# Performance work log

Measured on AMD Instinct MI355X. Metric: run time of the kernel, lower is better.

The kernel has to match this reference:

```python
import jax, jax.numpy as jnp
import numpy as np

B, C, T, D = 16, 1024, 2048, 512
EPS = 1e-5


def setup_inputs() -> dict:
    key = jax.random.key(0)
    ks = jax.random.split(key, 11)
    s_c = 1.0 / np.sqrt(C)
    s_d = 1.0 / np.sqrt(D)
    return {
        "x": jax.random.normal(ks[0], (B, C, T), dtype=jnp.float32),
        "Wq": jax.random.uniform(ks[1], (D, C), jnp.float32, -s_c, s_c),
        "bq": jax.random.uniform(ks[2], (D,), jnp.float32, -s_c, s_c),
        "Wk": jax.random.uniform(ks[3], (D, C), jnp.float32, -s_c, s_c),
        "bk": jax.random.uniform(ks[4], (D,), jnp.float32, -s_c, s_c),
        "Wv": jax.random.uniform(ks[5], (D, C), jnp.float32, -s_c, s_c),
        "bv": jax.random.uniform(ks[6], (D,), jnp.float32, -s_c, s_c),
        "Wo": jax.random.uniform(ks[7], (C, D), jnp.float32, -s_d, s_d),
        "bo": jax.random.uniform(ks[8], (C,), jnp.float32, -s_d, s_d),
        "gamma": jax.random.normal(ks[9], (C,), dtype=jnp.float32) * 0.1,
        "beta": jax.random.normal(ks[10], (C,), dtype=jnp.float32) * 0.1,
    }


def reference(x, Wq, bq, Wk, bk, Wv, bv, Wo, bo, gamma, beta):
    b, c, t = x.shape
    d = Wq.shape[0]
    # 1x1 Conv1d projections == channel-wise GEMMs
    q = jnp.einsum('dc,bct->btd', Wq, x) + bq            # (B, T, D)
    k = jnp.einsum('dc,bct->bdt', Wk, x) + bk[None, :, None]  # (B, D, T)
    v = jnp.einsum('dc,bct->bdt', Wv, x) + bv[None, :, None]  # (B, D, T)
    # sub_sample: MaxPool1d(kernel=2) on key/value along time
    k = k.reshape(b, d, t // 2, 2).max(axis=-1)          # (B, D, S)
    v = v.reshape(b, d, t // 2, 2).max(axis=-1)          # (B, D, S)
    # softmax-free attention: (Q @ K) / T then @ V
    attn = jnp.einsum('btd,bds->bts', q, k) / t          # (B, T, S)
    out = jnp.einsum('bts,bds->bdt', attn, v)            # (B, D, T)
    # output 1x1 conv
    y = jnp.einsum('cd,bdt->bct', Wo, out) + bo[None, :, None]  # (B, C, T)
    # BatchNorm1d (training-mode batch stats, biased variance)
    mu = y.mean(axis=(0, 2), keepdims=True)
    var = y.var(axis=(0, 2), keepdims=True)
    y = gamma[None, :, None] * (y - mu) * jax.lax.rsqrt(var + EPS) + beta[None, :, None]
    return y + x
```

## Files before the change

kernel.cpp:

```cpp
#include <hip/hip_runtime.h>

typedef unsigned short ushort_t;
typedef __bf16 bf16x8 __attribute__((ext_vector_type(8)));
typedef float floatx4 __attribute__((ext_vector_type(4)));
typedef ushort_t ushortx8 __attribute__((ext_vector_type(8)));

#define BM 128
#define BN 128
#define BKK 64

__device__ __forceinline__ ushort_t f2bf(float f) {
  union { float f; unsigned int u; } c; c.f = f;
  unsigned int r = c.u + 0x7FFFu + ((c.u >> 16) & 1u);
  return (ushort_t)(r >> 16);
}

__device__ __forceinline__ void async16(const ushort_t* g, ushort_t* l) {
  __builtin_amdgcn_global_load_lds(
      (const __attribute__((address_space(1))) unsigned int*)g,
      (__attribute__((address_space(3))) unsigned int*)l, 16, 0, 0);
}

template<int BIASM, int POOLM, bool OUTF32, bool STATS = false>
__global__ __launch_bounds__(512, 2)
void gemm256(const ushort_t* __restrict__ A, long aStr,
             const ushort_t* __restrict__ B, long bStr,
             void* __restrict__ Cp, long cStr,
             int K, int lda, int ldb, int ldc,
             const float* __restrict__ bias, float scale,
             float2* __restrict__ pstat = nullptr)
{
  __shared__ ushort_t As[2][256][64];
  __shared__ ushort_t Bs[2][256][64];
  __shared__ float2 part[4][256];

  A += (long)blockIdx.z * aStr;
  B += (long)blockIdx.z * bStr;
  float* Cf = (float*)Cp + (OUTF32 ? (long)blockIdx.z * cStr : 0);
  ushort_t* Cb = (ushort_t*)Cp + (OUTF32 ? 0 : (long)blockIdx.z * cStr);
  const int m0 = blockIdx.y * 256;
  const int n0 = blockIdx.x * 256;
  const int tid = threadIdx.x;
  const int lane = tid & 63;
  const int wid = tid >> 6;
  const int wm = wid >> 2;
  const int wn = wid & 3;
  const int l15 = lane & 15;
  const int lq  = lane >> 4;

  const int srow = tid >> 3;
  const int scb  = (((tid & 7) ^ (srow & 7)) << 3);
  const int dcb  = (tid & 7) << 3;

  const ushort_t* gA = A + (long)(m0 + srow) * lda + scb;
  const ushort_t* gB = B + (long)(n0 + srow) * ldb + scb;

  const int pb0 = ((lq ^ (l15 & 7)) << 3);
  const int pb1 = (((4 | lq) ^ (l15 & 7)) << 3);

  floatx4 acc[8][4];
#pragma unroll
  for (int i = 0; i < 8; ++i)
#pragma unroll
    for (int j = 0; j < 4; ++j)
#pragma unroll
      for (int r = 0; r < 4; ++r) acc[i][j][r] = 0.0f;

  bf16x8 aA[4][2], bB0[2][2], bB1[2][2];

  const int NT = K >> 6;
  const int NI = NT >> 1;

#define STAGE_A(sl, hf, kt) do { \
    const ushort_t* _s = gA + (long)((hf) * 128) * lda + ((kt) << 6); \
    async16(_s,                  &As[sl][(hf)*128      + srow][dcb]); \
    async16(_s + (long)64 * lda, &As[sl][(hf)*128 + 64 + srow][dcb]); \
  } while (0)
#define STAGE_B(sl, hf, kt) do { \
    const ushort_t* _s = gB + (long)((hf) * 128) * ldb + ((kt) << 6); \
    async16(_s,                  &Bs[sl][(hf)*128      + srow][dcb]); \
    async16(_s + (long)64 * ldb, &Bs[sl][(hf)*128 + 64 + srow][dcb]); \
  } while (0)
#define LD_A(sl, mh) do { \
    _Pragma("unroll") for (int _i = 0; _i < 4; ++_i) { \
      const int _r = wm*128 + (mh)*64 + _i*16 + l15; \
      aA[_i][0] = *(const bf16x8*)&As[sl][_r][pb0]; \
      aA[_i][1] = *(const bf16x8*)&As[sl][_r][pb1]; } \
  } while (0)
#define LD_B(sl, nh, dst) do { \
    _Pragma("unroll") for (int _j = 0; _j < 2; ++_j) { \
      const int _r = wn*64 + (nh)*32 + _j*16 + l15; \
      dst[_j][0] = *(const bf16x8*)&Bs[sl][_r][pb0]; \
      dst[_j][1] = *(const bf16x8*)&Bs[sl][_r][pb1]; } \
  } while (0)
#define MMA(mh, nh, bfr) do { \
    __builtin_amdgcn_s_setprio(1); \
    _Pragma("unroll") for (int _i = 0; _i < 4; ++_i) \
    _Pragma("unroll") for (int _j = 0; _j < 2; ++_j) { \
      floatx4& _c = acc[(mh)*4 + _i][(nh)*2 + _j]; \
      _c = __builtin_amdgcn_mfma_f32_16x16x32_bf16(aA[_i][0], (bfr)[_j][0], _c, 0, 0, 0); \
      _c = __builtin_amdgcn_mfma_f32_16x16x32_bf16(aA[_i][1], (bfr)[_j][1], _c, 0, 0, 0); } \
    __builtin_amdgcn_s_setprio(0); \
  } while (0)
#define SBAR  __builtin_amdgcn_s_barrier()
#define LGKM0 asm volatile("s_waitcnt lgkmcnt(0)" ::: "memory")
#define VM4   asm volatile("s_waitcnt vmcnt(4)" ::: "memory")
#define VM0   asm volatile("s_waitcnt vmcnt(0)" ::: "memory")

  STAGE_A(0, 0, 0); STAGE_A(0, 1, 0); STAGE_B(0, 0, 0); STAGE_B(0, 1, 0);
  STAGE_A(1, 0, 1); STAGE_B(1, 1, 1);
  VM4; SBAR;

  for (int i = 0; i < NI - 1; ++i) {
    const int t1 = 2*i + 1, t2 = 2*i + 2, t3 = 2*i + 3;
    LD_A(0, 0); LD_B(0, 0, bB0); STAGE_A(1, 1, t1);
    SBAR; LGKM0; MMA(0, 0, bB0); SBAR;
    LD_B(0, 1, bB1); STAGE_B(1, 0, t1);
    SBAR; LGKM0; MMA(0, 1, bB1); SBAR;
    LD_A(0, 1); STAGE_A(0, 0, t2);
    SBAR; LGKM0; MMA(1, 1, bB1); SBAR;
    STAGE_B(0, 1, t2);
    SBAR; LGKM0; MMA(1, 0, bB0); VM4; SBAR;
    LD_A(1, 0); LD_B(1, 0, bB0); STAGE_A(0, 1, t2);
    SBAR; LGKM0; MMA(0, 0, bB0); SBAR;
    LD_B(1, 1, bB1); STAGE_B(0, 0, t2);
    SBAR; LGKM0; MMA(0, 1, bB1); SBAR;
    LD_A(1, 1); STAGE_A(1, 0, t3);
    SBAR; LGKM0; MMA(1, 1, bB1); SBAR;
    STAGE_B(1, 1, t3);
    SBAR; LGKM0; MMA(1, 0, bB0); VM4; SBAR;
  }
  {
    const int t1 = NT - 1;
    LD_A(0, 0); LD_B(0, 0, bB0); STAGE_A(1, 1, t1);
    SBAR; LGKM0; MMA(0, 0, bB0); SBAR;
    LD_B(0, 1, bB1); STAGE_B(1, 0, t1);
    SBAR; LGKM0; MMA(0, 1, bB1); SBAR;
    LD_A(0, 1);
    SBAR; LGKM0; MMA(1, 1, bB1); SBAR;
    SBAR; LGKM0; MMA(1, 0, bB0); VM0; SBAR;
    LD_A(1, 0); LD_B(1, 0, bB0);
    SBAR; LGKM0; MMA(0, 0, bB0); SBAR;
    LD_B(1, 1, bB1);
    SBAR; LGKM0; MMA(0, 1, bB1); SBAR;
    LD_A(1, 1);
    SBAR; LGKM0; MMA(1, 1, bB1); SBAR;
    LGKM0; MMA(1, 0, bB0);
  }
#undef STAGE_A
#undef STAGE_B
#undef LD_A
#undef LD_B
#undef MMA
#undef SBAR
#undef LGKM0
#undef VM4
#undef VM0

#pragma unroll
  for (int mi = 0; mi < 8; ++mi) {
    const int mbase = m0 + wm*128 + (mi >> 2)*64 + (mi & 3)*16 + lq*4;
    float ss[4], ss2[4];
    if (STATS) {
#pragma unroll
      for (int r = 0; r < 4; ++r) { ss[r] = 0.0f; ss2[r] = 0.0f; }
    }
#pragma unroll
    for (int nj = 0; nj < 4; ++nj) {
      const int n = n0 + wn*64 + (nj >> 1)*32 + (nj & 1)*16 + l15;
      float v[4];
#pragma unroll
      for (int r = 0; r < 4; ++r) {
        v[r] = acc[mi][nj][r] * scale;
        if (BIASM == 1) v[r] += bias[mbase + r];
      }
      if (BIASM == 2) {
        const float bn_ = bias[n];
#pragma unroll
        for (int r = 0; r < 4; ++r) v[r] += bn_;
      }
      if (STATS) {
#pragma unroll
        for (int r = 0; r < 4; ++r) { ss[r] += v[r]; ss2[r] += v[r] * v[r]; }
      }
      if (POOLM == 0) {
#pragma unroll
        for (int r = 0; r < 4; ++r) {
          if (OUTF32) Cf[(long)(mbase + r) * ldc + n] = v[r];
          else        Cb[(long)(mbase + r) * ldc + n] = f2bf(v[r]);
        }
      } else if (POOLM == 1) {
#pragma unroll
        for (int r = 0; r < 4; ++r) {
          float o = __shfl_xor(v[r], 1);
          float w = fmaxf(v[r], o);
          if ((lane & 1) == 0) {
            if (OUTF32) Cf[(long)(mbase + r) * ldc + (n >> 1)] = w;
            else        Cb[(long)(mbase + r) * ldc + (n >> 1)] = f2bf(w);
          }
        }
      } else {
        float w0 = fmaxf(v[0], v[1]);
        float w1 = fmaxf(v[2], v[3]);
        const int mh = mbase >> 1;
        if (OUTF32) {
          Cf[(long)mh * ldc + n] = w0;
          Cf[(long)(mh + 1) * ldc + n] = w1;
        } else {
          Cb[(long)mh * ldc + n] = f2bf(w0);
          Cb[(long)(mh + 1) * ldc + n] = f2bf(w1);
        }
      }
    }
    if (STATS) {
#pragma unroll
      for (int o = 1; o < 16; o <<= 1) {
#pragma unroll
        for (int r = 0; r < 4; ++r) {
          ss[r]  += __shfl_xor(ss[r],  o);
          ss2[r] += __shfl_xor(ss2[r], o);
        }
      }
      if (l15 == 0) {
        const int chb = wm*128 + (mi >> 2)*64 + (mi & 3)*16 + lq*4;
#pragma unroll
        for (int r = 0; r < 4; ++r) part[wn][chb + r] = make_float2(ss[r], ss2[r]);
      }
    }
  }
  if (STATS) {
    __syncthreads();
    if (tid < 256) {
      float2 p0 = part[0][tid], p1 = part[1][tid], p2 = part[2][tid], p3 = part[3][tid];
      float2 p = make_float2(p0.x + p1.x + p2.x + p3.x, p0.y + p1.y + p2.y + p3.y);
      pstat[((long)blockIdx.z * gridDim.x + blockIdx.x) * 1024 + m0 + tid] = p;
    }
  }
}

template<int BIASM, int POOLM, bool OUTF32>
__global__ __launch_bounds__(256)
void gemm_bt(const ushort_t* __restrict__ A, long aStr,
             const ushort_t* __restrict__ B, long bStr,
             void* __restrict__ Cp, long cStr,
             int K, int lda, int ldb, int ldc,
             const float* __restrict__ bias, float scale)
{
  __shared__ ushort_t As[BM][BKK];
  __shared__ ushort_t Bs[BN][BKK];
  A += (long)blockIdx.z * aStr;
  B += (long)blockIdx.z * bStr;
  float* Cf = (float*)Cp + (OUTF32 ? (long)blockIdx.z * cStr : 0);
  ushort_t* Cb = (ushort_t*)Cp + (OUTF32 ? 0 : (long)blockIdx.z * cStr);
  const int m0 = blockIdx.y * BM;
  const int n0 = blockIdx.x * BN;
  const int tid = threadIdx.x;
  const int lane = tid & 63;
  const int wm = (tid >> 7) & 1;
  const int wn = (tid >> 6) & 1;
  const int ar = tid >> 3;
  const int ac = (tid & 7) * 8;

  floatx4 acc[4][4];
#pragma unroll
  for (int i = 0; i < 4; ++i)
#pragma unroll
    for (int j = 0; j < 4; ++j)
#pragma unroll
      for (int r = 0; r < 4; ++r) acc[i][j][r] = 0.0f;

  const int q8 = (lane >> 4) * 8;
  const int l15 = lane & 15;

  const ushort_t* gA = &A[(long)(m0 + ar) * lda + ac];
  const ushort_t* gB = &B[(long)(n0 + ar) * ldb + ac];
  const long aRow32 = (long)32 * lda;
  const long bRow32 = (long)32 * ldb;

  for (int k0 = 0; k0 < K; k0 += BKK) {
#pragma unroll
    for (int p = 0; p < 4; ++p)
      async16(gA + p * aRow32 + k0, &As[p * 32 + ar][ac]);
#pragma unroll
    for (int p = 0; p < 4; ++p)
      async16(gB + p * bRow32 + k0, &Bs[p * 32 + ar][ac]);
    __syncthreads();
#pragma unroll
    for (int kk = 0; kk < 2; ++kk) {
      const int kr = kk * 32 + q8;
      bf16x8 af[4], bfr[4];
#pragma unroll
      for (int i = 0; i < 4; ++i) {
        af[i]  = *(const bf16x8*)(&As[wm * 64 + i * 16 + l15][kr]);
        bfr[i] = *(const bf16x8*)(&Bs[wn * 64 + i * 16 + l15][kr]);
      }
#pragma unroll
      for (int i = 0; i < 4; ++i)
#pragma unroll
        for (int j = 0; j < 4; ++j)
          acc[i][j] = __builtin_amdgcn_mfma_f32_16x16x32_bf16(af[i], bfr[j], acc[i][j], 0, 0, 0);
    }
    __syncthreads();
  }

#pragma unroll
  for (int i = 0; i < 4; ++i) {
    const int mbase = m0 + wm * 64 + i * 16 + (lane >> 4) * 4;
#pragma unroll
    for (int j = 0; j < 4; ++j) {
      const int n = n0 + wn * 64 + j * 16 + l15;
      float v[4];
#pragma unroll
      for (int r = 0; r < 4; ++r) {
        v[r] = acc[i][j][r] * scale;
        if (BIASM == 1) v[r] += bias[mbase + r];
      }
      if (BIASM == 2) {
        const float bn_ = bias[n];
#pragma unroll
        for (int r = 0; r < 4; ++r) v[r] += bn_;
      }
      if (POOLM == 0) {
#pragma unroll
        for (int r = 0; r < 4; ++r) {
          if (OUTF32) Cf[(long)(mbase + r) * ldc + n] = v[r];
          else        Cb[(long)(mbase + r) * ldc + n] = f2bf(v[r]);
        }
      } else if (POOLM == 1) {
#pragma unroll
        for (int r = 0; r < 4; ++r) {
          float o = __shfl_xor(v[r], 1);
          float w = fmaxf(v[r], o);
          if ((lane & 1) == 0) {
            if (OUTF32) Cf[(long)(mbase + r) * ldc + (n >> 1)] = w;
            else        Cb[(long)(mbase + r) * ldc + (n >> 1)] = f2bf(w);
          }
        }
      } else {
        float w0 = fmaxf(v[0], v[1]);
        float w1 = fmaxf(v[2], v[3]);
        const int mh = mbase >> 1;
        if (OUTF32) {
          Cf[(long)mh * ldc + n] = w0;
          Cf[(long)(mh + 1) * ldc + n] = w1;
        } else {
          Cb[(long)mh * ldc + n] = f2bf(w0);
          Cb[(long)(mh + 1) * ldc + n] = f2bf(w1);
        }
      }
    }
  }
}

__global__ __launch_bounds__(256)
void transpose_f32_bf16(const float* __restrict__ src, ushort_t* __restrict__ dst,
                        int Rr, int Cl)
{
  __shared__ ushort_t tileT[64][72];
  const long boff = (long)blockIdx.z * Rr * Cl;
  const int t0 = blockIdx.x * 64;
  const int r0 = blockIdx.y * 64;
  const int tx = threadIdx.x & 15;
  const int ty = threadIdx.x >> 4;
#pragma unroll
  for (int i = 0; i < 4; ++i) {
    const int c = ty + 16 * i;
    floatx4 v = *(const floatx4*)&src[boff + (long)(r0 + c) * Cl + t0 + 4 * tx];
#pragma unroll
    for (int j = 0; j < 4; ++j) tileT[4 * tx + j][c] = f2bf(v[j]);
  }
  __syncthreads();
  const int cx = threadIdx.x & 7;
  const int tw = threadIdx.x >> 3;
#pragma unroll
  for (int i = 0; i < 2; ++i) {
    const int t = tw + 32 * i;
    ushortx8 w = *(const ushortx8*)&tileT[t][8 * cx];
    *(ushortx8*)&dst[boff + (long)(t0 + t) * Rr + r0 + 8 * cx] = w;
  }
}

__global__ __launch_bounds__(256)
void convert4(const float* __restrict__ a, const float* __restrict__ b,
              const float* __restrict__ c, const float* __restrict__ d,
              ushort_t* __restrict__ dst, int n,
              const float* __restrict__ bk, const float* __restrict__ bv,
              float* __restrict__ bkv)
{
  const float* srcs[4] = {a, b, c, d};
  const float* s = srcs[blockIdx.y];
  int i = blockIdx.x * 256 + threadIdx.x;
  if (i < n) dst[(long)blockIdx.y * n + i] = f2bf(s[i]);
  if (blockIdx.y == 0 && blockIdx.x == 0) {
    for (int j = threadIdx.x; j < 1024; j += 256)
      bkv[j] = (j < 512) ? bk[j] : bv[j - 512];
  }
}

__global__ __launch_bounds__(256)
void bn_apply(float* __restrict__ y, const float* __restrict__ x,
              const float2* __restrict__ pstat, const float* __restrict__ gamma,
              const float* __restrict__ beta)
{
  const int bc = blockIdx.x;
  const int c = bc & 1023;
  float s = 0.0f, s2 = 0.0f;
  if (threadIdx.x < 128) {
    float2 p = pstat[(long)threadIdx.x * 1024 + c];
    s = p.x; s2 = p.y;
  }
#pragma unroll
  for (int o = 32; o > 0; o >>= 1) { s += __shfl_down(s, o); s2 += __shfl_down(s2, o); }
  __shared__ float red[4];
  __shared__ float smv[2];
  const int w = threadIdx.x >> 6;
  if ((threadIdx.x & 63) == 0 && w < 2) { red[w] = s; red[2 + w] = s2; }
  __syncthreads();
  if (threadIdx.x == 0) {
    float ts = red[0] + red[1], ts2 = red[2] + red[3];
    const float inv = 1.0f / (16.0f * 2048.0f);
    float mean = ts * inv;
    float var = ts2 * inv - mean * mean;
    smv[0] = mean;
    smv[1] = rsqrtf(var + 1e-5f);
  }
  __syncthreads();
  const float mean = smv[0];
  const float g = gamma[c] * smv[1];
  const float bt = beta[c];
  const long off = (long)bc * 2048;
  floatx4* yp = (floatx4*)(y + off);
  const floatx4* xp = (const floatx4*)(x + off);
  for (int t = threadIdx.x; t < 512; t += 256) {
    floatx4 v = yp[t];
    floatx4 xv = xp[t];
#pragma unroll
    for (int r = 0; r < 4; ++r) v[r] = (v[r] - mean) * g + bt + xv[r];
    yp[t] = v;
  }
}

extern "C" void kernel_launch(void* const* d_in, const int* in_sizes, int n_in,
                              void* d_out, int out_size, void* d_ws, size_t ws_size,
                              hipStream_t stream) {
  (void)in_sizes; (void)n_in; (void)out_size; (void)ws_size;
  const float* x  = (const float*)d_in[0];
  const float* Wq = (const float*)d_in[1];
  const float* bq = (const float*)d_in[2];
  const float* Wk = (const float*)d_in[3];
  const float* bk = (const float*)d_in[4];
  const float* Wv = (const float*)d_in[5];
  const float* bv = (const float*)d_in[6];
  const float* Wo = (const float*)d_in[7];
  const float* bo = (const float*)d_in[8];
  const float* gamma = (const float*)d_in[9];
  const float* beta  = (const float*)d_in[10];
  float* out = (float*)d_out;

  const int Cc = 1024, T = 2048, D = 512, S = 1024;

  ushort_t* ws   = (ushort_t*)d_ws;
  ushort_t* xT   = ws;
  ushort_t* Qt   = ws + 33554432;
  ushort_t* KV   = ws + 50331648;
  ushort_t* WtT  = ws + 67108864;
  ushort_t* Wco  = ws + 71303168;
  ushort_t* Wq_b = ws + 79691776;
  ushort_t* Wo_b = ws + 79691776 + 3 * 524288;
  float*    bkv  = (float*)(ws + 81788928);
  float2*   pstat = (float2*)(ws + 81790976);

  dim3 blk(256);
  dim3 blk512(512);

  convert4<<<dim3(2048, 4), blk, 0, stream>>>(Wq, Wk, Wv, Wo, Wq_b, D * Cc,
                                              bk, bv, bkv);

  transpose_f32_bf16<<<dim3(T / 64, Cc / 64, 16), blk, 0, stream>>>(x, xT, Cc, T);

  gemm256<2, 0, false><<<dim3(D / 256, T / 256, 16), blk512, 0, stream>>>(
      xT, (long)T * Cc, Wq_b, 0, Qt, (long)T * D, Cc, Cc, Cc, D, bq, 1.0f);
  gemm256<1, 1, false><<<dim3(T / 256, 2 * D / 256, 16), blk512, 0, stream>>>(
      Wq_b + (long)D * Cc, 0, xT, (long)T * Cc, KV, (long)2 * D * S,
      Cc, Cc, Cc, S, bkv, 1.0f);

  gemm_bt<0, 0, false><<<dim3(D / 128, D / 128, 16), blk, 0, stream>>>(
      KV, (long)2 * D * S, KV + (long)D * S, (long)2 * D * S, WtT, (long)D * D,
      S, S, S, D, nullptr, 1.0f);
  gemm_bt<0, 0, false><<<dim3(D / 128, Cc / 128, 16), blk, 0, stream>>>(
      Wo_b, 0, WtT, (long)D * D, Wco, (long)Cc * D,
      D, D, D, D, nullptr, 1.0f / 2048.0f);

  gemm256<1, 0, true, true><<<dim3(T / 256, Cc / 256, 16), blk512, 0, stream>>>(
      Wco, (long)Cc * D, Qt, (long)T * D, out, (long)Cc * T,
      D, D, D, T, bo, 1.0f, pstat);

  bn_apply<<<dim3(16384), blk, 0, stream>>>(out, x, pstat, gamma, beta);
}
```

Measured before the change: 528.5 us.

## Merge Q/KV projection GEMMs into one launch and store pre-BN output as bf16

The Q projection and the pooled K/V projection now run in a single gemm_qkv launch. Block index picks the branch, and both branches share a factored-out gemm_core main loop. The output GEMM now writes its pre-BatchNorm result to a bf16 workspace buffer instead of f32 in the output tensor, while batch statistics are still taken from the f32 accumulators. bn_apply reads that bf16 buffer and writes the final f32 output, which cuts the traffic of the largest intermediate. The trade-off is extra rounding error from storing y in bf16 before normalization.

Measured after the change: 517.4 us. 2.1% less time.

```diff
diff --git a/kernel.cpp b/kernel.cpp
--- a/kernel.cpp
+++ b/kernel.cpp
@@ -4,6 +4,7 @@
 typedef __bf16 bf16x8 __attribute__((ext_vector_type(8)));
 typedef float floatx4 __attribute__((ext_vector_type(4)));
 typedef ushort_t ushortx8 __attribute__((ext_vector_type(8)));
+typedef ushort_t ushortx4 __attribute__((ext_vector_type(4)));
 
 #define BM 128
 #define BN 128
@@ -15,59 +16,26 @@
   return (ushort_t)(r >> 16);
 }
 
+__device__ __forceinline__ float bf2f(ushort_t u) {
+  union { unsigned int u; float f; } c; c.u = ((unsigned int)u) << 16;
+  return c.f;
+}
+
 __device__ __forceinline__ void async16(const ushort_t* g, ushort_t* l) {
   __builtin_amdgcn_global_load_lds(
       (const __attribute__((address_space(1))) unsigned int*)g,
       (__attribute__((address_space(3))) unsigned int*)l, 16, 0, 0);
 }
 
-template<int BIASM, int POOLM, bool OUTF32, bool STATS = false>
-__global__ __launch_bounds__(512, 2)
-void gemm256(const ushort_t* __restrict__ A, long aStr,
-             const ushort_t* __restrict__ B, long bStr,
-             void* __restrict__ Cp, long cStr,
-             int K, int lda, int ldb, int ldc,
-             const float* __restrict__ bias, float scale,
-             float2* __restrict__ pstat = nullptr)
-{
-  __shared__ ushort_t As[2][256][64];
-  __shared__ ushort_t Bs[2][256][64];
-  __shared__ float2 part[4][256];
-
-  A += (long)blockIdx.z * aStr;
-  B += (long)blockIdx.z * bStr;
-  float* Cf = (float*)Cp + (OUTF32 ? (long)blockIdx.z * cStr : 0);
-  ushort_t* Cb = (ushort_t*)Cp + (OUTF32 ? 0 : (long)blockIdx.z * cStr);
-  const int m0 = blockIdx.y * 256;
-  const int n0 = blockIdx.x * 256;
-  const int tid = threadIdx.x;
-  const int lane = tid & 63;
-  const int wid = tid >> 6;
-  const int wm = wid >> 2;
-  const int wn = wid & 3;
-  const int l15 = lane & 15;
-  const int lq  = lane >> 4;
-
-  const int srow = tid >> 3;
-  const int scb  = (((tid & 7) ^ (srow & 7)) << 3);
-  const int dcb  = (tid & 7) << 3;
-
-  const ushort_t* gA = A + (long)(m0 + srow) * lda + scb;
-  const ushort_t* gB = B + (long)(n0 + srow) * ldb + scb;
-
-  const int pb0 = ((lq ^ (l15 & 7)) << 3);
-  const int pb1 = (((4 | lq) ^ (l15 & 7)) << 3);
-
-  floatx4 acc[8][4];
-#pragma unroll
-  for (int i = 0; i < 8; ++i)
-#pragma unroll
-    for (int j = 0; j < 4; ++j)
-#pragma unroll
-      for (int r = 0; r < 4; ++r) acc[i][j][r] = 0.0f;
-
+__device__ __forceinline__ void gemm_core(
+    const ushort_t* __restrict__ gA, const ushort_t* __restrict__ gB,
+    int lda, int ldb, int K,
+    ushort_t (&As)[2][256][64], ushort_t (&Bs)[2][256][64],
+    const int srow, const int dcb, const int wm, const int wn,
+    const int l15, const int pb0, const int pb1,
+    floatx4 (&acc)[8][4])
+{
   bf16x8 aA[4][2], bB0[2][2], bB1[2][2];
-
   const int NT = K >> 6;
   const int NI = NT >> 1;
 
@@ -156,6 +124,52 @@
 #undef LGKM0
 #undef VM4
 #undef VM0
+}
+
+template<int BIASM, int POOLM, bool OUTF32, bool STATS = false>
+__global__ __launch_bounds__(512, 2)
+void gemm256(const ushort_t* __restrict__ A, long aStr,
+             const ushort_t* __restrict__ B, long bStr,
+             void* __restrict__ Cp, long cStr,
+             int K, int lda, int ldb, int ldc,
+             const float* __restrict__ bias, float scale,
+             float2* __restrict__ pstat = nullptr)
+{
+  __shared__ ushort_t As[2][256][64];
+  __shared__ ushort_t Bs[2][256][64];
+  __shared__ float2 part[4][256];
+
+  A += (long)blockIdx.z * aStr;
+  B += (long)blockIdx.z * bStr;
+  float* Cf = (float*)Cp + (OUTF32 ? (long)blockIdx.z * cStr : 0);
+  ushort_t* Cb = (ushort_t*)Cp + (OUTF32 ? 0 : (long)blockIdx.z * cStr);
+  const int m0 = blockIdx.y * 256;
+  const int n0 = blockIdx.x * 256;
+  const int tid = threadIdx.x;
+  const int lane = tid & 63;
+  const int wid = tid >> 6;
+  const int wm = wid >> 2;
+  const int wn = wid & 3;
+  const int l15 = lane & 15;
+  const int lq  = lane >> 4;
+  const int srow = tid >> 3;
+  const int scb  = (((tid & 7) ^ (srow & 7)) << 3);
+  const int dcb  = (tid & 7) << 3;
+  const int pb0 = ((lq ^ (l15 & 7)) << 3);
+  const int pb1 = (((4 | lq) ^ (l15 & 7)) << 3);
+
+  const ushort_t* gA = A + (long)(m0 + srow) * lda + scb;
+  const ushort_t* gB = B + (long)(n0 + srow) * ldb + scb;
+
+  floatx4 acc[8][4];
+#pragma unroll
+  for (int i = 0; i < 8; ++i)
+#pragma unroll
+    for (int j = 0; j < 4; ++j)
+#pragma unroll
+      for (int r = 0; r < 4; ++r) acc[i][j][r] = 0.0f;
+
+  gemm_core(gA, gB, lda, ldb, K, As, Bs, srow, dcb, wm, wn, l15, pb0, pb1, acc);
 
 #pragma unroll
   for (int mi = 0; mi < 8; ++mi) {
@@ -234,6 +248,86 @@
       float2 p0 = part[0][tid], p1 = part[1][tid], p2 = part[2][tid], p3 = part[3][tid];
       float2 p = make_float2(p0.x + p1.x + p2.x + p3.x, p0.y + p1.y + p2.y + p3.y);
       pstat[((long)blockIdx.z * gridDim.x + blockIdx.x) * 1024 + m0 + tid] = p;
+    }
+  }
+}
+
+__global__ __launch_bounds__(512, 2)
+void gemm_qkv(const ushort_t* __restrict__ xT, const ushort_t* __restrict__ Wq_b,
+              ushort_t* __restrict__ Qt, ushort_t* __restrict__ KV,
+              const float* __restrict__ bq, const float* __restrict__ bkv)
+{
+  __shared__ ushort_t As[2][256][64];
+  __shared__ ushort_t Bs[2][256][64];
+
+  const int z = blockIdx.z;
+  const int id = blockIdx.x;
+  const bool isQ = id < 16;
+  const int bx = isQ ? (id & 1) : ((id - 16) & 7);
+  const int by = isQ ? (id >> 1) : ((id - 16) >> 3);
+  const int m0 = by * 256;
+  const int n0 = bx * 256;
+  const ushort_t* xz = xT + (long)z * 2048 * 1024;
+  const ushort_t* Abase = isQ ? xz : (Wq_b + 512 * 1024);
+  const ushort_t* Bbase = isQ ? Wq_b : xz;
+
+  const int tid = threadIdx.x;
+  const int lane = tid & 63;
+  const int wid = tid >> 6;
+  const int wm = wid >> 2;
+  const int wn = wid & 3;
+  const int l15 = lane & 15;
+  const int lq  = lane >> 4;
+  const int srow = tid >> 3;
+  const int scb  = (((tid & 7) ^ (srow & 7)) << 3);
+  const int dcb  = (tid & 7) << 3;
+  const int pb0 = ((lq ^ (l15 & 7)) << 3);
+  const int pb1 = (((4 | lq) ^ (l15 & 7)) << 3);
+
+  const ushort_t* gA = Abase + (long)(m0 + srow) * 1024 + scb;
+  const ushort_t* gB = Bbase + (long)(n0 + srow) * 1024 + scb;
+
+  floatx4 acc[8][4];
+#pragma unroll
+  for (int i = 0; i < 8; ++i)
+#pragma unroll
+    for (int j = 0; j < 4; ++j)
+#pragma unroll
+      for (int r = 0; r < 4; ++r) acc[i][j][r] = 0.0f;
+
+  gemm_core(gA, gB, 1024, 1024, 1024, As, Bs, srow, dcb, wm, wn, l15, pb0, pb1, acc);
+
+  if (isQ) {
+    ushort_t* Cq = Qt + (long)z * 2048 * 512;
+#pragma unroll
+    for (int mi = 0; mi < 8; ++mi) {
+      const int mbase = m0 + wm*128 + (mi >> 2)*64 + (mi & 3)*16 + lq*4;
+#pragma unroll
+      for (int nj = 0; nj < 4; ++nj) {
+        const int n = n0 + wn*64 + (nj >> 1)*32 + (nj & 1)*16 + l15;
+        const float bn_ = bq[n];
+#pragma unroll
+        for (int r = 0; r < 4; ++r)
+          Cq[(long)(mbase + r) * 512 + n] = f2bf(acc[mi][nj][r] + bn_);
+      }
+    }
+  } else {
+    ushort_t* Ckv = KV + (long)z * 1024 * 1024;
+#pragma unroll
+    for (int mi = 0; mi < 8; ++mi) {
+      const int mbase = m0 + wm*128 + (mi >> 2)*64 + (mi & 3)*16 + lq*4;
+#pragma unroll
+      for (int nj = 0; nj < 4; ++nj) {
+        const int n = n0 + wn*64 + (nj >> 1)*32 + (nj & 1)*16 + l15;
+#pragma unroll
+        for (int r = 0; r < 4; ++r) {
+          float v = acc[mi][nj][r] + bkv[mbase + r];
+          float o = __shfl_xor(v, 1);
+          float w = fmaxf(v, o);
+          if ((lane & 1) == 0)
+            Ckv[(long)(mbase + r) * 1024 + (n >> 1)] = f2bf(w);
+        }
+      }
     }
   }
 }
@@ -398,9 +492,9 @@
 }
 
 __global__ __launch_bounds__(256)
-void bn_apply(float* __restrict__ y, const float* __restrict__ x,
-              const float2* __restrict__ pstat, const float* __restrict__ gamma,
-              const float* __restrict__ beta)
+void bn_apply(const ushort_t* __restrict__ yb, const float* __restrict__ x,
+              float* __restrict__ out, const float2* __restrict__ pstat,
+              const float* __restrict__ gamma, const float* __restrict__ beta)
 {
   const int bc = blockIdx.x;
   const int c = bc & 1023;
@@ -429,15 +523,19 @@
   const float g = gamma[c] * smv[1];
   const float bt = beta[c];
   const long off = (long)bc * 2048;
-  floatx4* yp = (floatx4*)(y + off);
+  const ushortx8* yp = (const ushortx8*)(yb + off);
   const floatx4* xp = (const floatx4*)(x + off);
-  for (int t = threadIdx.x; t < 512; t += 256) {
-    floatx4 v = yp[t];
-    floatx4 xv = xp[t];
-#pragma unroll
-    for (int r = 0; r < 4; ++r) v[r] = (v[r] - mean) * g + bt + xv[r];
-    yp[t] = v;
-  }
+  floatx4* op = (floatx4*)(out + off);
+  const int t = threadIdx.x;
+  ushortx8 v8 = yp[t];
+  floatx4 x0 = xp[2 * t], x1 = xp[2 * t + 1];
+  floatx4 o0, o1;
+#pragma unroll
+  for (int r = 0; r < 4; ++r) o0[r] = (bf2f(v8[r]) - mean) * g + bt + x0[r];
+#pragma unroll
+  for (int r = 0; r < 4; ++r) o1[r] = (bf2f(v8[4 + r]) - mean) * g + bt + x1[r];
+  op[2 * t] = o0;
+  op[2 * t + 1] = o1;
 }
 
 extern "C" void kernel_launch(void* const* d_in, const int* in_sizes, int n_in,
@@ -465,10 +563,11 @@
   ushort_t* KV   = ws + 50331648;
   ushort_t* WtT  = ws + 67108864;
   ushort_t* Wco  = ws + 71303168;
-  ushort_t* Wq_b = ws + 79691776;
-  ushort_t* Wo_b = ws + 79691776 + 3 * 524288;
-  float*    bkv  = (float*)(ws + 81788928);
-  float2*   pstat = (float2*)(ws + 81790976);
+  ushort_t* yb   = ws + 79691776;
+  ushort_t* Wq_b = ws + 113246208;
+  ushort_t* Wo_b = ws + 113246208 + 3 * 524288;
+  float*    bkv  = (float*)(ws + 115343360);
+  float2*   pstat = (float2*)(ws + 115345408);
 
   dim3 blk(256);
   dim3 blk512(512);
@@ -476,13 +575,9 @@
   convert4<<<dim3(2048, 4), blk, 0, stream>>>(Wq, Wk, Wv, Wo, Wq_b, D * Cc,
                                               bk, bv, bkv);
 
-  transpose_f32_bf16<<<dim3(T / 64, Cc / 64, 16), blk, 0, stream>>>(x, xT, Cc, T);
-
-  gemm256<2, 0, false><<<dim3(D / 256, T / 256, 16), blk512, 0, stream>>>(
-      xT, (long)T * Cc, Wq_b, 0, Qt, (long)T * D, Cc, Cc, Cc, D, bq, 1.0f);
-  gemm256<1, 1, false><<<dim3(T / 256, 2 * D / 256, 16), blk512, 0, stream>>>(
-      Wq_b + (long)D * Cc, 0, xT, (long)T * Cc, KV, (long)2 * D * S,
-      Cc, Cc, Cc, S, bkv, 1.0f);
+  transpose_f32_bf16<<<dim3(T / 32 / 2, Cc / 64, 16), blk, 0, stream>>>(x, xT, Cc, T);
+
+  gemm_qkv<<<dim3(48, 1, 16), blk512, 0, stream>>>(xT, Wq_b, Qt, KV, bq, bkv);
 
   gemm_bt<0, 0, false><<<dim3(D / 128, D / 128, 16), blk, 0, stream>>>(
       KV, (long)2 * D * S, KV + (long)D * S, (long)2 * D * S, WtT, (long)D * D,
@@ -491,9 +586,9 @@
       Wo_b, 0, WtT, (long)D * D, Wco, (long)Cc * D,
       D, D, D, D, nullptr, 1.0f / 2048.0f);
 
-  gemm256<1, 0, true, true><<<dim3(T / 256, Cc / 256, 16), blk512, 0, stream>>>(
-      Wco, (long)Cc * D, Qt, (long)T * D, out, (long)Cc * T,
+  gemm256<1, 0, false, true><<<dim3(T / 256, Cc / 256, 16), blk512, 0, stream>>>(
+      Wco, (long)Cc * D, Qt, (long)T * D, yb, (long)Cc * T,
       D, D, D, T, bo, 1.0f, pstat);
 
-  bn_apply<<<dim3(16384), blk, 0, stream>>>(out, x, pstat, gamma, beta);
-}
+  bn_apply<<<dim3(16384), blk, 0, stream>>>(yb, x, out, pstat, gamma, beta);
+}
```
